# Performance work log

Hardware: AMD Instinct MI355X
Metric: run time of the kernel (lower is better)

## Reference

```python
import jax, jax.numpy as jnp
import numpy as np

# NOTE: the original source calls an undefined selective_scan_fn(x, delta, A_bar, B_bar, C)
# and returns y_proj(y). We implement the standard S6 diagonal selective scan it implies:
#   h_t = A_bar_t * h_{t-1} + B_bar_t * u_t   (elementwise over latent dim, h_0 = 0)
#   y_t = C_t * h_t
# with u = x_proj(x) (the only use of the otherwise-dangling x_proj in the source).

IN_CH = 96
OUT_CH = 96
LATENT = 256
BATCH, H, W = 2, 128, 128


def _linear(x, w, b):
    return x @ w.T + b


def _s6(x, xw, xb, bcw, bcb, dw, db, yw, yb):
    # x: [B, L, Cin]
    u = _linear(x, xw, xb)                      # [B, L, D]
    bc = _linear(x, bcw, bcb)                   # [B, L, 2D]
    delta = _linear(x, dw, db)                  # [B, L, D]
    Bm, Cm = jnp.split(bc, 2, axis=-1)
    A_bar = jnp.exp(-jax.nn.softplus(delta))    # in (0, 1)
    B_bar = (1.0 - A_bar) * Bm
    elems = (A_bar, B_bar * u)

    def combine(c1, c2):
        a1, b1 = c1
        a2, b2 = c2
        return (a1 * a2, a2 * b1 + b2)

    _, h = jax.lax.associative_scan(combine, elems, axis=1)  # parallel scan over L
    y = Cm * h
    return _linear(y, yw, yb)                   # [B, L, D]


def setup_inputs() -> dict:
    key = jax.random.key(0)
    ks = jax.random.split(key, 16)
    s = 0.02
    inp = {
        "x": jax.random.normal(ks[0], (BATCH, IN_CH, H, W), jnp.float32),
        # S6 params (shared across all 4 directional scans, as in the source)
        "xw": jax.random.normal(ks[1], (LATENT, IN_CH), jnp.float32) * s,
        "xb": jnp.zeros((LATENT,), jnp.float32),
        "bcw": jax.random.normal(ks[2], (2 * LATENT, IN_CH), jnp.float32) * s,
        "bcb": jnp.zeros((2 * LATENT,), jnp.float32),
        "dw": jax.random.normal(ks[3], (LATENT, IN_CH), jnp.float32) * s,
        "db": jnp.zeros((LATENT,), jnp.float32),
        "yw": jax.random.normal(ks[4], (LATENT, LATENT), jnp.float32) * s,
        "yb": jnp.zeros((LATENT,), jnp.float32),
        # CrossMerge params
        "mw": jax.random.normal(ks[5], (LATENT, 4 * LATENT), jnp.float32) * s,
        "mb": jnp.zeros((LATENT,), jnp.float32),
        "gw": jax.random.normal(ks[6], (LATENT, 4 * LATENT), jnp.float32) * s,
        "gb": jnp.zeros((LATENT,), jnp.float32),
        "ow": jax.random.normal(ks[7], (OUT_CH, LATENT), jnp.float32) * s,
        "ob": jnp.zeros((OUT_CH,), jnp.float32),
    }
    return inp


def reference(x, xw, xb, bcw, bcb, dw, db, yw, yb, mw, mb, gw, gb, ow, ob):
    B, C, Hh, Ww = x.shape
    # cross_scan: 4 directional flattenings
    s1 = x.transpose(0, 2, 3, 1).reshape(B, Hh * Ww, C)   # 'b c h w -> b (h w) c'
    s2 = x.transpose(0, 3, 2, 1).reshape(B, Ww * Hh, C)   # 'b c h w -> b (w h) c'
    s3 = s1[:, ::-1, :]
    s4 = s2[:, ::-1, :]
    p = (xw, xb, bcw, bcb, dw, db, yw, yb)
    y1 = _s6(s1, *p)
    y2 = _s6(s2, *p)
    y3 = _s6(s3, *p)
    y4 = _s6(s4, *p)
    # CrossMerge
    y_cat = jnp.concatenate([y1, y2, y3, y4], axis=-1)    # [B, L, 4D]
    y_merged = _linear(y_cat, mw, mb)
    gate = jax.nn.sigmoid(_linear(y_cat, gw, gb))
    out = _linear(y_merged * gate, ow, ob)                # [B, L, OUT_CH]
    # 'b (h w) c -> b c h w'
    return out.reshape(B, Hh, Ww, -1).transpose(0, 3, 1, 2)
```

## Files before the change

### kernel.cpp

```cpp
#include <hip/hip_runtime.h>
#include <stdint.h>

#define LL 16384
#define NB 2
#define CIN 96
#define NLAT 256
#define COUT 96

typedef __attribute__((ext_vector_type(8))) short short8v;
typedef __attribute__((ext_vector_type(4))) float float4v;

__device__ __forceinline__ float b2f(unsigned short h) {
    return __uint_as_float(((unsigned int)h) << 16);
}
__device__ __forceinline__ unsigned short f2b(float f) {
    unsigned int u = __float_as_uint(f);
    unsigned int r = (u + 0x7FFFu + ((u >> 16) & 1u)) >> 16;
    return (unsigned short)r;
}

#define GLL16(g, s) __builtin_amdgcn_global_load_lds( \
    (const __attribute__((address_space(1))) unsigned int*)(g), \
    (__attribute__((address_space(3))) unsigned int*)(s), 16, 0, 0)

__global__ __launch_bounds__(256) void k_foldw_part(
    const float* __restrict__ yw, const float* __restrict__ mw, const float* __restrict__ gw,
    float* __restrict__ WF)
{
    __shared__ float At[64][68];
    __shared__ float Bt[64][68];
    int jt = blockIdx.x, nt = blockIdx.y, dzk = blockIdx.z;
    int kc = dzk & 3, dz = dzk >> 2;
    int d = dz & 3, mat = dz >> 2;
    const float* src = mat ? gw : mw;
    int j0 = jt * 64, n0 = nt * 64;
    int tid = threadIdx.x, tx = tid & 15, ty = tid >> 4;
    float acc[4][4] = {};
    int i0 = kc * 64;
    for (int rep = 0; rep < 16; ++rep) {
        int idx = rep * 256 + tid;
        int r = idx >> 6, cq = idx & 63;
        At[r][cq] = yw[(size_t)(i0 + r) * 256 + j0 + cq];
        Bt[cq][r] = src[(size_t)(n0 + r) * 1024 + d * 256 + i0 + cq];
    }
    __syncthreads();
    for (int ii = 0; ii < 64; ++ii) {
        float4 a4 = *(const float4*)(&At[ii][ty * 4]);
        float4 b4 = *(const float4*)(&Bt[ii][tx * 4]);
        float av[4] = {a4.x, a4.y, a4.z, a4.w};
        float bv[4] = {b4.x, b4.y, b4.z, b4.w};
        for (int q = 0; q < 4; ++q)
            for (int p = 0; p < 4; ++p)
                acc[q][p] = fmaf(av[q], bv[p], acc[q][p]);
    }
    float* dst = WF + (size_t)kc * 512 * 1024;
    for (int q = 0; q < 4; ++q) {
        int k = d * 256 + j0 + ty * 4 + q;
        for (int p = 0; p < 4; ++p) {
            int n = n0 + tx * 4 + p;
            dst[(size_t)(mat * 256 + n) * 1024 + k] = acc[q][p];
        }
    }
}

__global__ __launch_bounds__(256) void k_foldsum(
    const float* __restrict__ WF, unsigned short* __restrict__ WBT)
{
    int t = blockIdx.x * 256 + threadIdx.x;
    size_t o = (size_t)t * 4;
    const size_t S = (size_t)512 * 1024;
    float4 s0 = *(const float4*)(WF + o);
    float4 s1 = *(const float4*)(WF + S + o);
    float4 s2 = *(const float4*)(WF + 2 * S + o);
    float4 s3 = *(const float4*)(WF + 3 * S + o);
    unsigned short pk[4];
    pk[0] = f2b(s0.x + s1.x + s2.x + s3.x);
    pk[1] = f2b(s0.y + s1.y + s2.y + s3.y);
    pk[2] = f2b(s0.z + s1.z + s2.z + s3.z);
    pk[3] = f2b(s0.w + s1.w + s2.w + s3.w);
    *(unsigned long long*)(&WBT[o]) = *(const unsigned long long*)pk;
}

__global__ void k_foldbias(const float* __restrict__ mw, const float* __restrict__ gw,
                           const float* __restrict__ mb, const float* __restrict__ gb,
                           const float* __restrict__ yb,
                           float* __restrict__ bm2, float* __restrict__ bg2)
{
    int row = blockIdx.x;
    int lane = threadIdx.x;
    int n = row & 255;
    const float* W = (row < 256) ? mw : gw;
    float s = 0.f;
    for (int k = lane; k < 1024; k += 64)
        s = fmaf(W[(size_t)n * 1024 + k], yb[k & 255], s);
    for (int off = 32; off; off >>= 1) s += __shfl_down(s, off);
    if (lane == 0) {
        if (row < 256) bm2[n] = s + mb[n];
        else           bg2[n] = s + gb[n];
    }
}

__global__ __launch_bounds__(256) void k_xpose(
    const float* __restrict__ x, unsigned short* __restrict__ XT)
{
    int t = threadIdx.x;
    int p0 = blockIdx.x * 256;
    int b = p0 >> 14;
    int l = (p0 & (LL - 1)) + t;
    size_t gp = (size_t)(p0 + t);
    const float* xr = x + (size_t)b * 96 * LL + l;
    unsigned short* orow = XT + gp * 192;
#pragma unroll
    for (int kq = 0; kq < 12; ++kq) {
        short8v hi, lo;
#pragma unroll
        for (int c = 0; c < 8; ++c) {
            float v = xr[(size_t)(kq * 8 + c) * LL];
            unsigned short h = f2b(v);
            float r = v - b2f(h);
            hi[c] = (short)h;
            lo[c] = (short)f2b(r);
        }
        *(short8v*)(orow + kq * 8) = hi;
        *(short8v*)(orow + 96 + kq * 8) = lo;
    }
}

__global__ void k_wprep(
    const float* __restrict__ xw, const float* __restrict__ bcw, const float* __restrict__ dw,
    unsigned short* __restrict__ WPT)
{
    int rp = blockIdx.x * 32 + (threadIdx.x >> 3);
    int sub = threadIdx.x & 7;
    int nn16 = rp >> 6, g = (rp >> 4) & 3, ni = rp & 15;
    int n = nn16 * 16 + ni;
    const float* row;
    if (g == 0)      row = xw + (size_t)n * 96;
    else if (g == 1) row = bcw + (size_t)n * 96;
    else if (g == 2) row = bcw + (size_t)(256 + n) * 96;
    else             row = dw + (size_t)n * 96;
    unsigned short* orow = WPT + (size_t)rp * 192;
    for (int kq = sub; kq < 12; kq += 8) {
        short8v hv;
#pragma unroll
        for (int c = 0; c < 8; ++c) hv[c] = (short)f2b(row[kq * 8 + c]);
        *(short8v*)(orow + kq * 8) = hv;
        *(short8v*)(orow + 96 + kq * 8) = hv;
    }
}

__global__ void k_owprep(const float* __restrict__ ow, unsigned short* __restrict__ OWB)
{
    int r = blockIdx.x;
    int lane = threadIdx.x;
    unsigned short pk[4];
    if (r < 96) {
        float4 v = *(const float4*)(ow + (size_t)r * 256 + lane * 4);
        pk[0] = f2b(v.x); pk[1] = f2b(v.y); pk[2] = f2b(v.z); pk[3] = f2b(v.w);
    } else {
        pk[0] = pk[1] = pk[2] = pk[3] = 0;
    }
    *(unsigned long long*)(&OWB[(size_t)r * 256 + lane * 4]) = *(const unsigned long long*)pk;
}

__global__ __launch_bounds__(256) void k_proj_mfma(
    const unsigned short* __restrict__ XT, const unsigned short* __restrict__ WPT,
    const float* __restrict__ xb, const float* __restrict__ bcb, const float* __restrict__ db,
    unsigned int* __restrict__ AB, unsigned short* __restrict__ C)
{
    __shared__ __align__(16) unsigned short smA[128 * 32];
    __shared__ __align__(16) unsigned short smB[128 * 32];
    int tid = threadIdx.x;
    int w = tid >> 6, l = tid & 63;
    int mt = blockIdx.x;
    int bnt = blockIdx.y;
    int p0 = mt * 128;
    int bn0 = bnt * 128;

    int rowA = tid >> 2;
    int chA  = tid & 3;
    int laneRow = l & 15;
    int laneK   = l >> 4;

    float4v acc[2][8];
#pragma unroll
    for (int i = 0; i < 2; ++i)
#pragma unroll
        for (int f = 0; f < 8; ++f) acc[i][f] = (float4v)0.f;

    for (int kt = 0; kt < 6; ++kt) {
        const unsigned short* gA = XT + (size_t)(p0 + rowA) * 192 + kt * 32 + chA * 8;
        const unsigned short* gB = WPT + (size_t)(bn0 + rowA) * 192 + kt * 32 + chA * 8;
        GLL16(gA,            smA + tid * 8);
        GLL16(gA + 64 * 192, smA + 2048 + tid * 8);
        GLL16(gB,            smB + tid * 8);
        GLL16(gB + 64 * 192, smB + 2048 + tid * 8);
        __syncthreads();

        short8v a0 = *(const short8v*)(&smA[(w * 32 + laneRow) * 32 + laneK * 8]);
        short8v a1 = *(const short8v*)(&smA[(w * 32 + 16 + laneRow) * 32 + laneK * 8]);
#pragma unroll
        for (int f = 0; f < 8; ++f) {
            short8v bf_ = *(const short8v*)(&smB[(f * 16 + laneRow) * 32 + laneK * 8]);
            acc[0][f] = __builtin_amdgcn_mfma_f32_16x16x32_bf16(a0, bf_, acc[0][f], 0, 0, 0);
            acc[1][f] = __builtin_amdgcn_mfma_f32_16x16x32_bf16(a1, bf_, acc[1][f], 0, 0, 0);
        }
        __syncthreads();
    }

    int lr = l >> 4, lc = l & 15;
#pragma unroll
    for (int mr = 0; mr < 2; ++mr) {
#pragma unroll
        for (int nn2 = 0; nn2 < 2; ++nn2) {
            int n = (bnt * 2 + nn2) * 16 + lc;
            float xbv = xb[n], bb = bcb[n], cb = bcb[256 + n], dbv = db[n];
#pragma unroll
            for (int q = 0; q < 4; ++q) {
                int p = p0 + w * 32 + mr * 16 + lr * 4 + q;
                float u  = acc[mr][nn2 * 4 + 0][q] + xbv;
                float Bm = acc[mr][nn2 * 4 + 1][q] + bb;
                float Cm = acc[mr][nn2 * 4 + 2][q] + cb;
                float dl = acc[mr][nn2 * 4 + 3][q] + dbv;
                float a  = 1.0f / (1.0f + __expf(dl));
                float bu = (1.0f - a) * Bm * u;
                size_t base = (size_t)p * NLAT + n;
                AB[base] = (unsigned int)f2b(a) | ((unsigned int)f2b(bu) << 16);
                C[base]  = f2b(Cm);
            }
        }
    }
}

__device__ __forceinline__ int src_pos(int d, int t) {
    int s = (d >= 2) ? (LL - 1 - t) : t;
    return (d & 1) ? (((s & 127) << 7) | (s >> 7)) : s;
}

__global__ __launch_bounds__(256) void k_scan1(
    const unsigned int* __restrict__ AB,
    float* __restrict__ AggA, float* __restrict__ AggB)
{
    int n = threadIdx.x;
    int c = blockIdx.x, d = blockIdx.y, b = blockIdx.z;
    float h = 0.f, Ap = 1.f;
    int t0 = c * 256;
#pragma unroll 4
    for (int i = 0; i < 256; ++i) {
        int ls = src_pos(d, t0 + i);
        unsigned int v = AB[((size_t)b * LL + ls) * NLAT + n];
        float a  = __uint_as_float(v << 16);
        float bu = __uint_as_float(v & 0xFFFF0000u);
        h = fmaf(a, h, bu);
        Ap *= a;
    }
    size_t o = (((size_t)b * 4 + d) * 64 + c) * NLAT + n;
    AggA[o] = Ap; AggB[o] = h;
}

__global__ void k_scan2(const float* __restrict__ AggA, const float* __restrict__ AggB,
                        float* __restrict__ Hs)
{
    int n = threadIdx.x;
    int d = blockIdx.x, b = blockIdx.y;
    float h = 0.f;
    for (int c = 0; c < 64; ++c) {
        size_t o = (((size_t)b * 4 + d) * 64 + c) * NLAT + n;
        Hs[o] = h;
        h = fmaf(AggA[o], h, AggB[o]);
    }
}

__global__ __launch_bounds__(256) void k_scan3(
    const unsigned int* __restrict__ AB, const unsigned short* __restrict__ C,
    const float* __restrict__ Hs, unsigned short* __restrict__ ys)
{
    int n = threadIdx.x;
    int c = blockIdx.x, d = blockIdx.y, b = blockIdx.z;
    size_t o = (((size_t)b * 4 + d) * 64 + c) * NLAT + n;
    float h = Hs[o];
    int t0 = c * 256;
    size_t ybase = (((size_t)b * 4 + d) * LL + t0) * NLAT + n;
#pragma unroll 4
    for (int i = 0; i < 256; ++i) {
        int ls = src_pos(d, t0 + i);
        size_t idx = ((size_t)b * LL + ls) * NLAT + n;
        unsigned int v = AB[idx];
        float a  = __uint_as_float(v << 16);
        float bu = __uint_as_float(v & 0xFFFF0000u);
        h = fmaf(a, h, bu);
        float y = b2f(C[idx]) * h;
        ys[ybase + (size_t)i * NLAT] = f2b(y);
    }
}

__global__ __launch_bounds__(256) void k_merge_mfma(
    const unsigned short* __restrict__ ys,
    const unsigned short* __restrict__ WBT,
    const float* __restrict__ bm2, const float* __restrict__ bg2,
    unsigned short* __restrict__ z)
{
    __shared__ __align__(16) unsigned short smA[128 * 32];
    __shared__ __align__(16) unsigned short smB[128 * 32];
    int tid = threadIdx.x;
    int w = tid >> 6, l = tid & 63;
    int mt = blockIdx.x;
    int nt = blockIdx.y;
    int p0 = mt * 128;
    int b4 = (p0 >> 14) * 4;
    int l0 = p0 & (LL - 1);
    int n0 = nt * 64;

    int rowA = tid >> 2;
    int chA  = tid & 3;
    int laneRow = l & 15;
    int laneK   = l >> 4;

    float4v accM[2][4], accG[2][4];
#pragma unroll
    for (int i = 0; i < 2; ++i)
#pragma unroll
        for (int j = 0; j < 4; ++j) { accM[i][j] = (float4v)0.f; accG[i][j] = (float4v)0.f; }

    for (int kt = 0; kt < 32; ++kt) {
        int d = kt >> 3;
        int j0k = (kt & 7) * 32;
        const unsigned short* gA = ys + (((size_t)(b4 + d)) * LL + l0 + rowA) * 256 + j0k + chA * 8;
        const unsigned short* gB = WBT + ((size_t)(n0 + rowA)) * 1024 + kt * 32 + chA * 8;
        GLL16(gA,              smA + tid * 8);
        GLL16(gA + 64 * 256,   smA + 2048 + tid * 8);
        GLL16(gB,              smB + tid * 8);
        GLL16(gB + 256 * 1024, smB + 2048 + tid * 8);
        __syncthreads();

        short8v a0 = *(const short8v*)(&smA[(w * 32 + laneRow) * 32 + laneK * 8]);
        short8v a1 = *(const short8v*)(&smA[(w * 32 + 16 + laneRow) * 32 + laneK * 8]);
#pragma unroll
        for (int nr = 0; nr < 4; ++nr) {
            short8v bm_ = *(const short8v*)(&smB[(nr * 16 + laneRow) * 32 + laneK * 8]);
            short8v bg_ = *(const short8v*)(&smB[(64 + nr * 16 + laneRow) * 32 + laneK * 8]);
            accM[0][nr] = __builtin_amdgcn_mfma_f32_16x16x32_bf16(a0, bm_, accM[0][nr], 0, 0, 0);
            accM[1][nr] = __builtin_amdgcn_mfma_f32_16x16x32_bf16(a1, bm_, accM[1][nr], 0, 0, 0);
            accG[0][nr] = __builtin_amdgcn_mfma_f32_16x16x32_bf16(a0, bg_, accG[0][nr], 0, 0, 0);
            accG[1][nr] = __builtin_amdgcn_mfma_f32_16x16x32_bf16(a1, bg_, accG[1][nr], 0, 0, 0);
        }
        __syncthreads();
    }

    int lr = l >> 4, lc = l & 15;
#pragma unroll
    for (int mr = 0; mr < 2; ++mr) {
#pragma unroll
        for (int nr = 0; nr < 4; ++nr) {
            int n = n0 + nr * 16 + lc;
            float bmv = bm2[n], bgv = bg2[n];
#pragma unroll
            for (int q = 0; q < 4; ++q) {
                int p = p0 + w * 32 + mr * 16 + lr * 4 + q;
                float m = accM[mr][nr][q] + bmv;
                float g = accG[mr][nr][q] + bgv;
                float zv = m / (1.f + __expf(-g));
                z[(size_t)p * NLAT + n] = f2b(zv);
            }
        }
    }
}

__global__ __launch_bounds__(256) void k_out_mfma(
    const unsigned short* __restrict__ z, const unsigned short* __restrict__ OWB,
    const float* __restrict__ ob, float* __restrict__ out)
{
    __shared__ __align__(16) unsigned short smA[128 * 32];
    __shared__ __align__(16) unsigned short smB[128 * 32];
    int tid = threadIdx.x;
    int w = tid >> 6, l = tid & 63;
    int p0 = blockIdx.x * 128;
    int b = p0 >> 14;
    int l0 = p0 & (LL - 1);

    int rowA = tid >> 2;
    int chA  = tid & 3;
    int laneRow = l & 15;
    int laneK   = l >> 4;

    float4v acc[2][6];
#pragma unroll
    for (int i = 0; i < 2; ++i)
#pragma unroll
        for (int f = 0; f < 6; ++f) acc[i][f] = (float4v)0.f;

    for (int kt = 0; kt < 8; ++kt) {
        const unsigned short* gA = z + (size_t)(p0 + rowA) * 256 + kt * 32 + chA * 8;
        const unsigned short* gB = OWB + (size_t)rowA * 256 + kt * 32 + chA * 8;
        GLL16(gA,            smA + tid * 8);
        GLL16(gA + 64 * 256, smA + 2048 + tid * 8);
        GLL16(gB,            smB + tid * 8);
        GLL16(gB + 64 * 256, smB + 2048 + tid * 8);
        __syncthreads();

        short8v a0 = *(const short8v*)(&smA[(w * 32 + laneRow) * 32 + laneK * 8]);
        short8v a1 = *(const short8v*)(&smA[(w * 32 + 16 + laneRow) * 32 + laneK * 8]);
#pragma unroll
        for (int nr = 0; nr < 6; ++nr) {
            short8v bf_ = *(const short8v*)(&smB[(nr * 16 + laneRow) * 32 + laneK * 8]);
            acc[0][nr] = __builtin_amdgcn_mfma_f32_16x16x32_bf16(a0, bf_, acc[0][nr], 0, 0, 0);
            acc[1][nr] = __builtin_amdgcn_mfma_f32_16x16x32_bf16(a1, bf_, acc[1][nr], 0, 0, 0);
        }
        __syncthreads();
    }

    int lr = l >> 4, lc = l & 15;
#pragma unroll
    for (int mr = 0; mr < 2; ++mr) {
#pragma unroll
        for (int nr = 0; nr < 6; ++nr) {
            int c = nr * 16 + lc;
            float obv = ob[c];
            int ll = l0 + w * 32 + mr * 16 + lr * 4;
            float4 v;
            v.x = acc[mr][nr][0] + obv;
            v.y = acc[mr][nr][1] + obv;
            v.z = acc[mr][nr][2] + obv;
            v.w = acc[mr][nr][3] + obv;
            *(float4*)(&out[((size_t)(b * 96 + c)) * LL + ll]) = v;
        }
    }
}

extern "C" void kernel_launch(void* const* d_in, const int* in_sizes, int n_in,
                              void* d_out, int out_size, void* d_ws, size_t ws_size,
                              hipStream_t stream) {
    (void)in_sizes; (void)n_in; (void)out_size; (void)ws_size;
    const float* x   = (const float*)d_in[0];
    const float* xw  = (const float*)d_in[1];
    const float* xb  = (const float*)d_in[2];
    const float* bcw = (const float*)d_in[3];
    const float* bcb = (const float*)d_in[4];
    const float* dw  = (const float*)d_in[5];
    const float* db  = (const float*)d_in[6];
    const float* yw  = (const float*)d_in[7];
    const float* yb  = (const float*)d_in[8];
    const float* mw  = (const float*)d_in[9];
    const float* mb  = (const float*)d_in[10];
    const float* gw  = (const float*)d_in[11];
    const float* gb  = (const float*)d_in[12];
    const float* ow  = (const float*)d_in[13];
    const float* ob  = (const float*)d_in[14];
    float* out = (float*)d_out;

    char* ws = (char*)d_ws;
    size_t off = 0;
    auto alloc = [&](size_t bytes) -> void* {
        void* p = ws + off;
        off += (bytes + 255) & ~(size_t)255;
        return p;
    };
    unsigned int*   AB  = (unsigned int*)  alloc((size_t)NB * LL * NLAT * 4);
    unsigned short* C   = (unsigned short*)alloc((size_t)NB * LL * NLAT * 2);
    unsigned short* YS  = (unsigned short*)alloc((size_t)NB * 4 * LL * NLAT * 2);
    unsigned short* Z   = (unsigned short*)alloc((size_t)NB * LL * NLAT * 2);
    unsigned short* WBT = (unsigned short*)alloc((size_t)512 * 1024 * 2);
    unsigned short* XT  = (unsigned short*)alloc((size_t)NB * LL * 192 * 2);
    unsigned short* WPT = (unsigned short*)alloc((size_t)1024 * 192 * 2);
    unsigned short* OWB = (unsigned short*)alloc((size_t)128 * 256 * 2);
    float* WF   = (float*)alloc((size_t)4 * 512 * 1024 * 4);
    float* BM2  = (float*)alloc(256 * 4);
    float* BG2  = (float*)alloc(256 * 4);
    float* AggA = (float*)alloc((size_t)NB * 4 * 64 * NLAT * 4);
    float* AggB = (float*)alloc((size_t)NB * 4 * 64 * NLAT * 4);
    float* HS   = (float*)alloc((size_t)NB * 4 * 64 * NLAT * 4);

    k_foldw_part<<<dim3(4, 4, 32),  256, 0, stream>>>(yw, mw, gw, WF);
    k_foldsum   <<<512,             256, 0, stream>>>(WF, WBT);
    k_foldbias  <<<512,              64, 0, stream>>>(mw, gw, mb, gb, yb, BM2, BG2);
    k_wprep     <<<32,              256, 0, stream>>>(xw, bcw, dw, WPT);
    k_owprep    <<<128,              64, 0, stream>>>(ow, OWB);
    k_xpose     <<<128,             256, 0, stream>>>(x, XT);
    k_proj_mfma <<<dim3(256, 8),    256, 0, stream>>>(XT, WPT, xb, bcb, db, AB, C);
    k_scan1     <<<dim3(64, 4, NB), 256, 0, stream>>>(AB, AggA, AggB);
    k_scan2     <<<dim3(4, NB),     256, 0, stream>>>(AggA, AggB, HS);
    k_scan3     <<<dim3(64, 4, NB), 256, 0, stream>>>(AB, C, HS, YS);
    k_merge_mfma<<<dim3(256, 4),    256, 0, stream>>>(YS, WBT, BM2, BG2, Z);
    k_out_mfma  <<<256,             256, 0, stream>>>(Z, OWB, ob, out);
}
```

Baseline: 200.8 us.

## Widen merge GEMM K-tile with XOR-swizzled LDS and split transpose across warps

```diff
diff --git a/kernel.cpp b/kernel.cpp
--- a/kernel.cpp
+++ b/kernel.cpp
@@ -104,14 +104,17 @@
     const float* __restrict__ x, unsigned short* __restrict__ XT)
 {
     int t = threadIdx.x;
-    int p0 = blockIdx.x * 256;
+    int pl = t & 63;
+    int grp = t >> 6;
+    int p0 = blockIdx.x * 64;
     int b = p0 >> 14;
-    int l = (p0 & (LL - 1)) + t;
-    size_t gp = (size_t)(p0 + t);
+    int l = (p0 & (LL - 1)) + pl;
+    size_t gp = (size_t)(p0 + pl);
     const float* xr = x + (size_t)b * 96 * LL + l;
     unsigned short* orow = XT + gp * 192;
 #pragma unroll
-    for (int kq = 0; kq < 12; ++kq) {
+    for (int kk = 0; kk < 3; ++kk) {
+        int kq = grp * 3 + kk;
         short8v hi, lo;
 #pragma unroll
         for (int c = 0; c < 8; ++c) {
@@ -300,8 +303,8 @@
     const float* __restrict__ bm2, const float* __restrict__ bg2,
     unsigned short* __restrict__ z)
 {
-    __shared__ __align__(16) unsigned short smA[128 * 32];
-    __shared__ __align__(16) unsigned short smB[128 * 32];
+    __shared__ __align__(16) unsigned short smA[128 * 64];
+    __shared__ __align__(16) unsigned short smB[128 * 64];
     int tid = threadIdx.x;
     int w = tid >> 6, l = tid & 63;
     int mt = blockIdx.x;
@@ -311,10 +314,11 @@
     int l0 = p0 & (LL - 1);
     int n0 = nt * 64;
 
-    int rowA = tid >> 2;
-    int chA  = tid & 3;
+    int rowS = tid >> 3;
+    int cg   = (tid & 7) ^ (rowS & 7);
     int laneRow = l & 15;
     int laneK   = l >> 4;
+    int rx8 = (laneRow & 7);
 
     float4v accM[2][4], accG[2][4];
 #pragma unroll
@@ -322,27 +326,36 @@
 #pragma unroll
         for (int j = 0; j < 4; ++j) { accM[i][j] = (float4v)0.f; accG[i][j] = (float4v)0.f; }
 
-    for (int kt = 0; kt < 32; ++kt) {
-        int d = kt >> 3;
-        int j0k = (kt & 7) * 32;
-        const unsigned short* gA = ys + (((size_t)(b4 + d)) * LL + l0 + rowA) * 256 + j0k + chA * 8;
-        const unsigned short* gB = WBT + ((size_t)(n0 + rowA)) * 1024 + kt * 32 + chA * 8;
-        GLL16(gA,              smA + tid * 8);
-        GLL16(gA + 64 * 256,   smA + 2048 + tid * 8);
-        GLL16(gB,              smB + tid * 8);
-        GLL16(gB + 256 * 1024, smB + 2048 + tid * 8);
-        __syncthreads();
-
-        short8v a0 = *(const short8v*)(&smA[(w * 32 + laneRow) * 32 + laneK * 8]);
-        short8v a1 = *(const short8v*)(&smA[(w * 32 + 16 + laneRow) * 32 + laneK * 8]);
-#pragma unroll
-        for (int nr = 0; nr < 4; ++nr) {
-            short8v bm_ = *(const short8v*)(&smB[(nr * 16 + laneRow) * 32 + laneK * 8]);
-            short8v bg_ = *(const short8v*)(&smB[(64 + nr * 16 + laneRow) * 32 + laneK * 8]);
-            accM[0][nr] = __builtin_amdgcn_mfma_f32_16x16x32_bf16(a0, bm_, accM[0][nr], 0, 0, 0);
-            accM[1][nr] = __builtin_amdgcn_mfma_f32_16x16x32_bf16(a1, bm_, accM[1][nr], 0, 0, 0);
-            accG[0][nr] = __builtin_amdgcn_mfma_f32_16x16x32_bf16(a0, bg_, accG[0][nr], 0, 0, 0);
-            accG[1][nr] = __builtin_amdgcn_mfma_f32_16x16x32_bf16(a1, bg_, accG[1][nr], 0, 0, 0);
+    for (int kt = 0; kt < 16; ++kt) {
+        int d = kt >> 2;
+        int j0k = (kt & 3) * 64;
+        const unsigned short* gAb = ys + (((size_t)(b4 + d)) * LL + l0) * 256 + j0k + cg * 8;
+#pragma unroll
+        for (int rep = 0; rep < 4; ++rep) {
+            GLL16(gAb + (size_t)(rep * 32 + rowS) * 256, smA + rep * 2048 + tid * 8);
+        }
+#pragma unroll
+        for (int rep = 0; rep < 4; ++rep) {
+            int rr = rep * 32 + rowS;
+            int nrow = (rr < 64) ? (n0 + rr) : (256 + n0 + rr - 64);
+            GLL16(WBT + (size_t)nrow * 1024 + kt * 64 + cg * 8, smB + rep * 2048 + tid * 8);
+        }
+        __syncthreads();
+
+#pragma unroll
+        for (int ksub = 0; ksub < 2; ++ksub) {
+            int cxo = ((ksub * 4 + laneK) ^ rx8) * 8;
+            short8v a0 = *(const short8v*)(&smA[(w * 32 + laneRow) * 64 + cxo]);
+            short8v a1 = *(const short8v*)(&smA[(w * 32 + 16 + laneRow) * 64 + cxo]);
+#pragma unroll
+            for (int nr = 0; nr < 4; ++nr) {
+                short8v bm_ = *(const short8v*)(&smB[(nr * 16 + laneRow) * 64 + cxo]);
+                short8v bg_ = *(const short8v*)(&smB[(64 + nr * 16 + laneRow) * 64 + cxo]);
+                accM[0][nr] = __builtin_amdgcn_mfma_f32_16x16x32_bf16(a0, bm_, accM[0][nr], 0, 0, 0);
+                accM[1][nr] = __builtin_amdgcn_mfma_f32_16x16x32_bf16(a1, bm_, accM[1][nr], 0, 0, 0);
+                accG[0][nr] = __builtin_amdgcn_mfma_f32_16x16x32_bf16(a0, bg_, accG[0][nr], 0, 0, 0);
+                accG[1][nr] = __builtin_amdgcn_mfma_f32_16x16x32_bf16(a1, bg_, accG[1][nr], 0, 0, 0);
+            }
         }
         __syncthreads();
     }
@@ -475,7 +488,7 @@
     k_foldbias  <<<512,              64, 0, stream>>>(mw, gw, mb, gb, yb, BM2, BG2);
     k_wprep     <<<32,              256, 0, stream>>>(xw, bcw, dw, WPT);
     k_owprep    <<<128,              64, 0, stream>>>(ow, OWB);
-    k_xpose     <<<128,             256, 0, stream>>>(x, XT);
+    k_xpose     <<<512,             256, 0, stream>>>(x, XT);
     k_proj_mfma <<<dim3(256, 8),    256, 0, stream>>>(XT, WPT, xb, bcb, db, AB, C);
     k_scan1     <<<dim3(64, 4, NB), 256, 0, stream>>>(AB, AggA, AggB);
     k_scan2     <<<dim3(4, NB),     256, 0, stream>>>(AggA, AggB, HS);
```

Result: no change. 198.3 us (-1.3%).
